# Kernel optimization log

Measured on AMD Instinct MI355X. Metric: run time of the kernel, lower is better.

The kernel has to match this reference:

```python
import jax, jax.numpy as jnp
import numpy as np

B, T, D, E, V, EXTRA = 32, 1024, 512, 256, 50257, 200


def setup_inputs() -> dict:
    key = jax.random.key(0)
    ks = jax.random.split(key, 20)
    s = 0.02
    rn = lambda k, shape: jax.random.normal(k, shape, dtype=jnp.float32) * s
    inp = {}
    inp["decoder_input"] = jax.random.randint(ks[0], (B,), 0, V)
    inp["h0"] = rn(ks[1], (B, D))
    inp["c0"] = rn(ks[2], (B, D))
    inp["encoder_outputs"] = rn(ks[3], (B, T, 2 * D))
    inp["encoder_pad_mask"] = jnp.ones((B, T), jnp.float32)
    inp["previous_context_vector"] = rn(ks[4], (B, 2 * D))
    inp["coverage"] = jax.random.uniform(ks[5], (B, T), jnp.float32) * 0.01
    inp["extra_zeros"] = jnp.zeros((B, EXTRA), jnp.float32)
    inp["encoder_input_extra_vocabs"] = jax.random.randint(ks[6], (B, T), 0, V + EXTRA)
    inp["step"] = 1
    inp["embedding"] = rn(ks[7], (V, E))
    inp["W_gx"] = rn(ks[8], (2 * D + E, E)); inp["b_gx"] = jnp.zeros((E,), jnp.float32)
    inp["W_ih"] = rn(ks[9], (E, 4 * D)); inp["W_hh"] = rn(ks[10], (D, 4 * D))
    inp["b_ih"] = jnp.zeros((4 * D,), jnp.float32); inp["b_hh"] = jnp.zeros((4 * D,), jnp.float32)
    inp["W_h"] = rn(ks[11], (2 * D, 2 * D))
    inp["W_c"] = rn(ks[12], (2 * D,))
    inp["W_s"] = rn(ks[13], (2 * D, 2 * D)); inp["b_s"] = jnp.zeros((2 * D,), jnp.float32)
    inp["v"] = rn(ks[14], (2 * D,))
    inp["W_pg"] = rn(ks[15], (4 * D + E,)); inp["b_pg"] = jnp.zeros((1,), jnp.float32)
    inp["W_v1"] = rn(ks[16], (3 * D, D)); inp["b_v1"] = jnp.zeros((D,), jnp.float32)
    inp["W_v2"] = rn(ks[17], (D, V)); inp["b_v2"] = jnp.zeros((V,), jnp.float32)
    return inp


def reference(decoder_input, h0, c0, encoder_outputs, encoder_pad_mask,
              previous_context_vector, coverage, extra_zeros,
              encoder_input_extra_vocabs, step,
              embedding, W_gx, b_gx, W_ih, W_hh, b_ih, b_hh,
              W_h, W_c, W_s, b_s, v, W_pg, b_pg, W_v1, b_v1, W_v2, b_v2):
    # Pointer-generator decoder single step (training path / step>0), coverage on.
    softmax_temperature = 1.0
    emb = embedding[decoder_input]                                  # [B,E]
    x = jnp.concatenate([previous_context_vector, emb], -1) @ W_gx + b_gx  # [B,E]
    # LSTM cell, torch gate order (i, f, g, o)
    gates = x @ W_ih + h0 @ W_hh + b_ih + b_hh                      # [B,4D]
    i, f, g, o = jnp.split(gates, 4, axis=-1)
    c1 = jax.nn.sigmoid(f) * c0 + jax.nn.sigmoid(i) * jnp.tanh(g)
    h1 = jax.nn.sigmoid(o) * jnp.tanh(c1)                           # [B,D]
    dec_hat = jnp.concatenate([h1, c1], -1)                         # [B,2D]
    # Bahdanau additive attention with coverage feature
    enc_feat = encoder_outputs @ W_h                                # [B,T,2D]
    dec_feat = dec_hat @ W_s + b_s                                  # [B,2D]
    cov_feat = coverage[..., None] * W_c                            # [B,T,2D]
    energy = jnp.tanh(enc_feat + dec_feat[:, None, :] + cov_feat)
    scores = energy @ v                                             # [B,T]
    att = jax.nn.softmax(scores / softmax_temperature, axis=-1) * encoder_pad_mask
    att = att / att.sum(-1, keepdims=True)                          # renormalized
    context = jnp.einsum('bt,btd->bd', att, encoder_outputs)        # [B,2D]
    coverage_next = coverage + att
    # pointer-generator gate
    pg_in = jnp.concatenate([context, dec_hat, x], -1)              # [B,4D+E]
    p_gen = jax.nn.sigmoid(pg_in @ W_pg + b_pg)[:, None]            # [B,1]
    out = jnp.concatenate([h1, context], -1)                        # [B,3D]
    logits = ((out @ W_v1 + b_v1) @ W_v2 + b_v2) / softmax_temperature
    vocab_dist = jax.nn.softmax(logits, axis=-1)                    # [B,V]
    vd_oov = jnp.concatenate([p_gen * vocab_dist, extra_zeros], 1)  # [B,V+EXTRA]
    att_oov = (1.0 - p_gen) * att                                   # [B,T]
    rows = jnp.arange(B)[:, None]
    vocab_dist_final = vd_oov.at[rows, encoder_input_extra_vocabs].add(att_oov)
    return (vocab_dist_final, (h1, c1), context, att, coverage_next)
```

## Files before the change

kernel.cpp:

```cpp
#include <hip/hip_runtime.h>
#include <hip/hip_bf16.h>

typedef __attribute__((ext_vector_type(4))) float f32x4;
typedef __attribute__((ext_vector_type(8))) short s16x8;
typedef __attribute__((ext_vector_type(4))) short s16x4;

#define DEVINL __device__ __forceinline__

static constexpr int BB = 32, TT = 1024, DD = 512, EE = 256, VV = 50257, EXTRA = 200;
static constexpr int D2 = 1024;
static constexpr int VE = VV + EXTRA;
static constexpr long MM = (long)BB * TT;
static constexpr int NBLK = 786;

DEVINL unsigned short f2bf(float x) {
    union { float f; unsigned int u; } c; c.f = x;
    unsigned int u = c.u;
    u += 0x7fffu + ((u >> 16) & 1u);
    return (unsigned short)(u >> 16);
}
DEVINL float bf2f(unsigned short h) {
    union { unsigned int u; float f; } c; c.u = ((unsigned int)h) << 16;
    return c.f;
}
DEVINL float sigmoidf_(float x) { return 1.0f / (1.0f + __expf(-x)); }
DEVINL float tanh_fast(float x) {
    x = fminf(15.f, fmaxf(-15.f, x));
    float e = __expf(2.f * x);
    return (e - 1.f) / (e + 1.f);
}
DEVINL void gl16(const void* g, void* l) {
    __builtin_amdgcn_global_load_lds((__attribute__((address_space(1))) void*)g,
                                     (__attribute__((address_space(3))) void*)l, 16, 0, 0);
}

__global__ __launch_bounds__(256) void k_prep(const float* __restrict__ Wh,
                                              const float* __restrict__ enc,
                                              unsigned short* __restrict__ WhT,
                                              unsigned short* __restrict__ encswz) {
    __shared__ float tile[32][33];
    const int bid = blockIdx.x, tid = threadIdx.x;
    if (bid < 1024) {
        int n0 = (bid & 31) * 32, k0 = (bid >> 5) * 32;
        int col = tid & 31, row = tid >> 5;
        #pragma unroll
        for (int i = 0; i < 4; i++)
            tile[row + i * 8][col] = Wh[(long)(k0 + row + i * 8) * D2 + n0 + col];
        __syncthreads();
        #pragma unroll
        for (int i = 0; i < 4; i++) {
            int n = n0 + row + i * 8;
            int kcol = (k0 + col) ^ ((n & 7) << 3);
            WhT[(long)n * D2 + kcol] = f2bf(tile[col][row + i * 8]);
        }
    } else {
        long idx = (long)(bid - 1024) * 256 + tid;
        int m  = (int)(idx >> 7);
        int k2 = (int)(idx & 127) * 8;
        int s  = (m & 7) << 3;
        const float* src = enc + (long)m * 1024 + (k2 ^ s);
        f32x4 a = *(const f32x4*)src;
        f32x4 b = *(const f32x4*)(src + 4);
        s16x8 h;
        h[0] = (short)f2bf(a[0]); h[1] = (short)f2bf(a[1]); h[2] = (short)f2bf(a[2]); h[3] = (short)f2bf(a[3]);
        h[4] = (short)f2bf(b[0]); h[5] = (short)f2bf(b[1]); h[6] = (short)f2bf(b[2]); h[7] = (short)f2bf(b[3]);
        *(s16x8*)(encswz + (long)m * 1024 + k2) = h;
    }
}

__global__ __launch_bounds__(512) void k_x(
    const int* __restrict__ dec_in, const float* __restrict__ pcv,
    const float* __restrict__ embt, const float* __restrict__ Wgx,
    const float* __restrict__ bgx, float* __restrict__ xbuf) {
    __shared__ float xs[1280];
    __shared__ float sred[8][64];
    int b = blockIdx.x, n0 = blockIdx.y * 64;
    int tid = threadIdx.x, nl = tid & 63, ks = tid >> 6;
    long er = (long)dec_in[b] * EE;
    for (int i = tid; i < 1280; i += 512)
        xs[i] = (i < 1024) ? pcv[b * 1024 + i] : embt[er + i - 1024];
    __syncthreads();
    float acc = 0.f;
    for (int k = ks * 160; k < ks * 160 + 160; ++k)
        acc += xs[k] * Wgx[(long)k * EE + n0 + nl];
    sred[ks][nl] = acc;
    __syncthreads();
    if (tid < 64) {
        int n = n0 + tid;
        float s = bgx[n];
        #pragma unroll
        for (int i = 0; i < 8; i++) s += sred[i][tid];
        xbuf[b * EE + n] = s;
    }
}

__global__ __launch_bounds__(512) void k_lstm(
    const float* __restrict__ xbuf, const float* __restrict__ h0,
    const float* __restrict__ c0, const float* __restrict__ Wih,
    const float* __restrict__ Whh, const float* __restrict__ bih,
    const float* __restrict__ bhh, float* __restrict__ h1o,
    float* __restrict__ c1o, float* __restrict__ dechat) {
    __shared__ float xs[768];
    __shared__ float sred[4][8][64];
    int b = blockIdx.x, d0 = blockIdx.y * 64;
    int tid = threadIdx.x, dl = tid & 63, ks = tid >> 6;
    for (int i = tid; i < 768; i += 512)
        xs[i] = (i < 256) ? xbuf[b * 256 + i] : h0[b * 512 + i - 256];
    __syncthreads();
    float a0 = 0, a1 = 0, a2 = 0, a3 = 0;
    for (int k = ks * 96; k < ks * 96 + 96; ++k) {
        float xv = xs[k];
        const float* wr = (k < 256) ? (Wih + (long)k * 2048) : (Whh + (long)(k - 256) * 2048);
        a0 += xv * wr[d0 + dl];        a1 += xv * wr[512 + d0 + dl];
        a2 += xv * wr[1024 + d0 + dl]; a3 += xv * wr[1536 + d0 + dl];
    }
    sred[0][ks][dl] = a0; sred[1][ks][dl] = a1; sred[2][ks][dl] = a2; sred[3][ks][dl] = a3;
    __syncthreads();
    if (tid < 64) {
        int d = d0 + tid;
        float gi = bih[d] + bhh[d];
        float gf = bih[512 + d] + bhh[512 + d];
        float gg = bih[1024 + d] + bhh[1024 + d];
        float go = bih[1536 + d] + bhh[1536 + d];
        #pragma unroll
        for (int s = 0; s < 8; s++) {
            gi += sred[0][s][tid]; gf += sred[1][s][tid];
            gg += sred[2][s][tid]; go += sred[3][s][tid];
        }
        float c1 = sigmoidf_(gf) * c0[b * 512 + d] + sigmoidf_(gi) * tanh_fast(gg);
        float h1 = sigmoidf_(go) * tanh_fast(c1);
        h1o[b * 512 + d] = h1; c1o[b * 512 + d] = c1;
        dechat[b * 1024 + d] = h1; dechat[b * 1024 + 512 + d] = c1;
    }
}

__global__ __launch_bounds__(512) void k_decfeat(
    const float* __restrict__ dechat, const float* __restrict__ Ws,
    const float* __restrict__ bs, float* __restrict__ decfeat) {
    __shared__ float xs[1024];
    __shared__ float sred[8][64];
    int b = blockIdx.x, n0 = blockIdx.y * 64;
    int tid = threadIdx.x, nl = tid & 63, ks = tid >> 6;
    for (int i = tid; i < 1024; i += 512) xs[i] = dechat[b * 1024 + i];
    __syncthreads();
    float acc = 0.f;
    for (int k = ks * 128; k < ks * 128 + 128; ++k)
        acc += xs[k] * Ws[(long)k * 1024 + n0 + nl];
    sred[ks][nl] = acc;
    __syncthreads();
    if (tid < 64) {
        int n = n0 + tid;
        float s = bs[n];
        #pragma unroll
        for (int i = 0; i < 8; i++) s += sred[i][tid];
        decfeat[b * 1024 + n] = s;
    }
}

__global__ __launch_bounds__(512) void k_scores(
    const unsigned short* __restrict__ encswz, const unsigned short* __restrict__ whtswz,
    const float* __restrict__ decfeat, const float* __restrict__ cov,
    const float* __restrict__ Wc, const float* __restrict__ vvec,
    float* __restrict__ scorep) {
    __shared__ __align__(16) unsigned short As[128 * 64];
    __shared__ __align__(16) unsigned short Bs[256 * 64];
    __shared__ float sred[4][128];
    const int tid = threadIdx.x;
    const int lane = tid & 63, wave = tid >> 6;
    const int wid = __builtin_amdgcn_readfirstlane(wave);
    const int g = lane >> 4, c = lane & 15;
    const int wm = wave >> 2, wn = wave & 3;

    const int bid = blockIdx.x;
    const int xcd = bid & 7, t = bid >> 3;
    const int mt = xcd * 32 + (t >> 2), nt = t & 3;
    const long m0 = (long)mt * 128;
    const int n0 = nt * 256;
    const int bblk = mt >> 3;

    const int arow = wid * 16 + (lane >> 3);
    const int axo  = (lane & 7) * 8;
    const int brow = wid * 32 + (lane >> 3);
    unsigned short* aBase = &As[wid * 1024];
    unsigned short* bBase = &Bs[wid * 2048];

    f32x4 acc[4][4];
    #pragma unroll
    for (int i = 0; i < 4; i++)
        #pragma unroll
        for (int j = 0; j < 4; j++) acc[i][j] = (f32x4){0.f, 0.f, 0.f, 0.f};

    const int sx = (c & 7) << 3;

    for (int kt = 0; kt < 16; ++kt) {
        const int k0 = kt * 64;
        __syncthreads();
        gl16(encswz + (m0 + arow) * 1024 + k0 + axo,       aBase);
        gl16(encswz + (m0 + arow + 8) * 1024 + k0 + axo,   aBase + 512);
        gl16(whtswz + (long)(n0 + brow) * 1024 + k0 + axo,        bBase);
        gl16(whtswz + (long)(n0 + brow + 8) * 1024 + k0 + axo,    bBase + 512);
        gl16(whtswz + (long)(n0 + brow + 16) * 1024 + k0 + axo,   bBase + 1024);
        gl16(whtswz + (long)(n0 + brow + 24) * 1024 + k0 + axo,   bBase + 1536);
        __syncthreads();
        #pragma unroll
        for (int kk = 0; kk < 2; ++kk) {
            const int kse = (kk * 32 + g * 8) ^ sx;
            s16x8 af[4], bfj[4];
            #pragma unroll
            for (int i = 0; i < 4; i++) af[i] = *(const s16x8*)&As[(wm * 64 + i * 16 + c) * 64 + kse];
            #pragma unroll
            for (int j = 0; j < 4; j++) bfj[j] = *(const s16x8*)&Bs[(wn * 64 + j * 16 + c) * 64 + kse];
            #pragma unroll
            for (int i = 0; i < 4; i++)
                #pragma unroll
                for (int j = 0; j < 4; j++)
                    acc[i][j] = __builtin_amdgcn_mfma_f32_16x16x32_bf16(af[i], bfj[j], acc[i][j], 0, 0, 0);
        }
    }
    float dfv[4], wcv[4], vvj[4];
    #pragma unroll
    for (int j = 0; j < 4; j++) {
        int col = n0 + wn * 64 + j * 16 + c;
        dfv[j] = decfeat[bblk * D2 + col];
        wcv[j] = Wc[col];
        vvj[j] = vvec[col];
    }
    float sAcc[4][4];
    #pragma unroll
    for (int i = 0; i < 4; i++) {
        #pragma unroll
        for (int r = 0; r < 4; r++) {
            const long m = m0 + wm * 64 + i * 16 + g * 4 + r;
            const float covm = cov[m];
            float su = 0.f;
            #pragma unroll
            for (int j = 0; j < 4; j++) {
                float e = acc[i][j][r] + dfv[j] + covm * wcv[j];
                su += tanh_fast(e) * vvj[j];
            }
            su += __shfl_xor(su, 1); su += __shfl_xor(su, 2);
            su += __shfl_xor(su, 4); su += __shfl_xor(su, 8);
            sAcc[i][r] = su;
        }
    }
    if (c == 0) {
        #pragma unroll
        for (int i = 0; i < 4; i++)
            #pragma unroll
            for (int r = 0; r < 4; r++)
                sred[wn][wm * 64 + i * 16 + g * 4 + r] = sAcc[i][r];
    }
    __syncthreads();
    if (tid < 128)
        scorep[(long)nt * MM + m0 + tid] = sred[0][tid] + sred[1][tid] + sred[2][tid] + sred[3][tid];
}

__global__ __launch_bounds__(256) void k_ctx(
    const float* __restrict__ scorep, const float* __restrict__ mask,
    const float* __restrict__ cov, const unsigned short* __restrict__ encswz,
    float* __restrict__ att, float* __restrict__ covn, float* __restrict__ part) {
    int b = blockIdx.x, tc = blockIdx.y;
    int tid = threadIdx.x;
    __shared__ float sm[8];
    __shared__ float attL[1024];
    float sv[4];
    float mx = -1e30f;
    #pragma unroll
    for (int i = 0; i < 4; i++) {
        long idx = (long)b * TT + tid + 256 * i;
        sv[i] = scorep[idx] + scorep[MM + idx] + scorep[2 * MM + idx] + scorep[3 * MM + idx];
        mx = fmaxf(mx, sv[i]);
    }
    for (int o = 32; o; o >>= 1) mx = fmaxf(mx, __shfl_xor(mx, o));
    if ((tid & 63) == 0) sm[tid >> 6] = mx;
    __syncthreads();
    mx = fmaxf(fmaxf(sm[0], sm[1]), fmaxf(sm[2], sm[3]));
    __syncthreads();
    float e[4]; float s = 0.f;
    #pragma unroll
    for (int i = 0; i < 4; i++) { e[i] = __expf(sv[i] - mx); s += e[i]; }
    for (int o = 32; o; o >>= 1) s += __shfl_xor(s, o);
    if ((tid & 63) == 0) sm[tid >> 6] = s;
    __syncthreads();
    s = sm[0] + sm[1] + sm[2] + sm[3];
    __syncthreads();
    float inv = 1.f / s;
    float am[4]; float s2 = 0.f;
    #pragma unroll
    for (int i = 0; i < 4; i++) { am[i] = e[i] * inv * mask[b * TT + tid + 256 * i]; s2 += am[i]; }
    for (int o = 32; o; o >>= 1) s2 += __shfl_xor(s2, o);
    if ((tid & 63) == 0) sm[tid >> 6] = s2;
    __syncthreads();
    s2 = sm[0] + sm[1] + sm[2] + sm[3];
    float inv2 = 1.f / s2;
    #pragma unroll
    for (int i = 0; i < 4; i++) {
        int t = tid + 256 * i;
        float a = am[i] * inv2;
        attL[t] = a;
        if (tc == 0) {
            att[b * TT + t] = a;
            covn[b * TT + t] = cov[b * TT + t] + a;
        }
    }
    __syncthreads();
    int d8 = (tid & 127) * 8;
    int tofs = tid >> 7;
    float a0 = 0, a1 = 0, a2 = 0, a3 = 0, a4 = 0, a5 = 0, a6 = 0, a7 = 0;
    for (int t = tc * 64 + tofs; t < tc * 64 + 64; t += 2) {
        float a = attL[t];
        int sx = (t & 7) << 3;
        const unsigned short* ep = encswz + ((long)b * TT + t) * D2 + (d8 ^ sx);
        s16x8 ev = *(const s16x8*)ep;
        a0 += a * bf2f((unsigned short)ev[0]); a1 += a * bf2f((unsigned short)ev[1]);
        a2 += a * bf2f((unsigned short)ev[2]); a3 += a * bf2f((unsigned short)ev[3]);
        a4 += a * bf2f((unsigned short)ev[4]); a5 += a * bf2f((unsigned short)ev[5]);
        a6 += a * bf2f((unsigned short)ev[6]); a7 += a * bf2f((unsigned short)ev[7]);
    }
    float* pp = part + (long)(tc * 2 + tofs) * BB * D2 + b * D2 + d8;
    pp[0] = a0; pp[1] = a1; pp[2] = a2; pp[3] = a3;
    pp[4] = a4; pp[5] = a5; pp[6] = a6; pp[7] = a7;
}

__global__ __launch_bounds__(512) void k_hidden2(
    const float* __restrict__ part, const float* __restrict__ h1,
    const float* __restrict__ dechat, const float* __restrict__ xbuf,
    const float* __restrict__ Wpg, const float* __restrict__ bpg,
    const float* __restrict__ Wv1, const float* __restrict__ bv1,
    float* __restrict__ ctx, float* __restrict__ pgen,
    unsigned short* __restrict__ hbf) {
    __shared__ float xs[1536];
    __shared__ float sred[8][64];
    int b = blockIdx.x, n0 = blockIdx.y * 64;
    int tid = threadIdx.x, nl = tid & 63, ks = tid >> 6;
    for (int i = tid; i < 512; i += 512) xs[i] = h1[b * 512 + i];
    #pragma unroll
    for (int d = tid; d < 1024; d += 512) {
        float s = 0.f;
        #pragma unroll
        for (int p = 0; p < 32; p++) s += part[(long)p * BB * D2 + b * D2 + d];
        xs[512 + d] = s;
        if (blockIdx.y == 0) ctx[b * D2 + d] = s;
    }
    __syncthreads();
    if (blockIdx.y == 0) {
        float pacc = xs[512 + tid] * Wpg[tid] + dechat[b * D2 + tid] * Wpg[D2 + tid]
                   + xs[1024 + tid] * Wpg[512 + tid] + dechat[b * D2 + 512 + tid] * Wpg[D2 + 512 + tid];
        if (tid < EE) pacc += xbuf[b * EE + tid] * Wpg[2 * D2 + tid];
        for (int o = 32; o; o >>= 1) pacc += __shfl_xor(pacc, o);
        if ((tid & 63) == 0) sred[7][(tid >> 6) + 8] = 0.f;
        __shared__ float psum[8];
        if ((tid & 63) == 0) psum[tid >> 6] = pacc;
        __syncthreads();
        if (tid == 0) {
            float t = 0.f;
            #pragma unroll
            for (int i = 0; i < 8; i++) t += psum[i];
            pgen[b] = sigmoidf_(t + bpg[0]);
        }
        __syncthreads();
    }
    float acc = 0.f;
    for (int k = ks * 192; k < ks * 192 + 192; ++k)
        acc += xs[k] * Wv1[(long)k * 512 + n0 + nl];
    sred[ks][nl] = acc;
    __syncthreads();
    if (tid < 64) {
        int n = n0 + tid;
        float s = bv1[n];
        #pragma unroll
        for (int i = 0; i < 8; i++) s += sred[i][tid];
        hbf[b * 512 + n] = f2bf(s);
    }
}

__global__ __launch_bounds__(256) void k_logits(const unsigned short* __restrict__ hbf,
                                                const float* __restrict__ Wv2,
                                                const float* __restrict__ bv2,
                                                float* __restrict__ logits,
                                                float* __restrict__ bsm,
                                                float* __restrict__ bss) {
    constexpr int PITCH = 136;
    __shared__ __align__(16) unsigned short Bs[64 * PITCH];
    __shared__ float sm_[4][16], ss_[4][16];
    const int tid = threadIdx.x;
    const int lane = tid & 63, wave = tid >> 6;
    const int g = lane >> 4, c = lane & 15;
    const int wm = wave >> 1, wn = wave & 1;
    const long v0 = (long)blockIdx.x * 64;
    const bool tail = (v0 + 64 > VV);

    const int vg = tid & 15, kr = tid >> 4;

    f32x4 acc[2];
    acc[0] = (f32x4){0.f, 0.f, 0.f, 0.f};
    acc[1] = (f32x4){0.f, 0.f, 0.f, 0.f};
    const int sxr = (c & 7) << 3;

    f32x4 wa[4], wb[4];
    #pragma unroll
    for (int pi = 0; pi < 4; ++pi) {
        const int ka = kr * 8 + pi * 2;
        if (!tail) {
            wa[pi] = *(const f32x4*)&Wv2[(long)ka * VV + v0 + vg * 4];
            wb[pi] = *(const f32x4*)&Wv2[(long)(ka + 1) * VV + v0 + vg * 4];
        } else {
            #pragma unroll
            for (int j = 0; j < 4; j++) {
                long v = v0 + vg * 4 + j;
                long vs = (v < VV) ? v : (VV - 1);
                wa[pi][j] = Wv2[(long)ka * VV + vs];
                wb[pi][j] = Wv2[(long)(ka + 1) * VV + vs];
            }
        }
    }
    #pragma unroll
    for (int kt = 0; kt < 4; ++kt) {
        const int k0 = kt * 128;
        __syncthreads();
        #pragma unroll
        for (int pi = 0; pi < 4; ++pi) {
            #pragma unroll
            for (int j = 0; j < 4; j++) {
                int vl = vg * 4 + j;
                int ks = (kr * 8 + pi * 2) ^ ((vl & 7) << 3);
                unsigned int pack = (unsigned int)f2bf(wa[pi][j]) | ((unsigned int)f2bf(wb[pi][j]) << 16);
                *(unsigned int*)&Bs[vl * PITCH + ks] = pack;
            }
        }
        if (kt < 3) {
            const int k1 = (kt + 1) * 128;
            #pragma unroll
            for (int pi = 0; pi < 4; ++pi) {
                const int ka = k1 + kr * 8 + pi * 2;
                if (!tail) {
                    wa[pi] = *(const f32x4*)&Wv2[(long)ka * VV + v0 + vg * 4];
                    wb[pi] = *(const f32x4*)&Wv2[(long)(ka + 1) * VV + v0 + vg * 4];
                } else {
                    #pragma unroll
                    for (int j = 0; j < 4; j++) {
                        long v = v0 + vg * 4 + j;
                        long vs = (v < VV) ? v : (VV - 1);
                        wa[pi][j] = Wv2[(long)ka * VV + vs];
                        wb[pi][j] = Wv2[(long)(ka + 1) * VV + vs];
                    }
                }
            }
        }
        __syncthreads();
        #pragma unroll
        for (int kk = 0; kk < 4; ++kk) {
            const int koff = kk * 32 + g * 8;
            const int kse = koff ^ sxr;
            s16x8 af = *(const s16x8*)&hbf[(wm * 16 + c) * 512 + k0 + koff];
            s16x8 bf0 = *(const s16x8*)&Bs[(wn * 32 + c) * PITCH + kse];
            s16x8 bf1 = *(const s16x8*)&Bs[(wn * 32 + 16 + c) * PITCH + kse];
            acc[0] = __builtin_amdgcn_mfma_f32_16x16x32_bf16(af, bf0, acc[0], 0, 0, 0);
            acc[1] = __builtin_amdgcn_mfma_f32_16x16x32_bf16(af, bf1, acc[1], 0, 0, 0);
        }
    }
    float lv[2][4];
    #pragma unroll
    for (int j = 0; j < 2; j++) {
        long v = v0 + wn * 32 + j * 16 + c;
        bool valid = (v < VV);
        float bvv = valid ? bv2[v] : 0.f;
        #pragma unroll
        for (int r = 0; r < 4; r++) {
            float val = acc[j][r] + bvv;
            if (valid) {
                int b = wm * 16 + g * 4 + r;
                logits[(long)b * VV + v] = val;
                lv[j][r] = val;
            } else {
                lv[j][r] = -1e30f;
            }
        }
    }
    float mrow[4], srow[4];
    #pragma unroll
    for (int r = 0; r < 4; r++) {
        float m = fmaxf(lv[0][r], lv[1][r]);
        m = fmaxf(m, __shfl_xor(m, 1)); m = fmaxf(m, __shfl_xor(m, 2));
        m = fmaxf(m, __shfl_xor(m, 4)); m = fmaxf(m, __shfl_xor(m, 8));
        float s = __expf(lv[0][r] - m) + __expf(lv[1][r] - m);
        s += __shfl_xor(s, 1); s += __shfl_xor(s, 2);
        s += __shfl_xor(s, 4); s += __shfl_xor(s, 8);
        mrow[r] = m; srow[r] = s;
    }
    if (c == 0) {
        #pragma unroll
        for (int r = 0; r < 4; r++) { sm_[wave][g * 4 + r] = mrow[r]; ss_[wave][g * 4 + r] = srow[r]; }
    }
    __syncthreads();
    if (tid < 32) {
        int b = tid;
        int w0 = (b >> 4) * 2, ridx = b & 15;
        float mA = sm_[w0][ridx], mB = sm_[w0 + 1][ridx];
        float sA = ss_[w0][ridx], sB = ss_[w0 + 1][ridx];
        float m = fmaxf(mA, mB);
        float s = sA * __expf(mA - m) + sB * __expf(mB - m);
        bsm[(long)b * NBLK + blockIdx.x] = m;
        bss[(long)b * NBLK + blockIdx.x] = s;
    }
}

__global__ __launch_bounds__(512) void k_vocab(
    const float* __restrict__ logits, const float* __restrict__ bsm,
    const float* __restrict__ bss, const float* __restrict__ pgen,
    const float* __restrict__ extraz, float* __restrict__ out0) {
    int b = blockIdx.x;
    int v0 = blockIdx.y * 2048;
    int tid = threadIdx.x;
    __shared__ float smm[8], sms[8], fin[2];
    float m = -1e30f, s = 0.f;
    #pragma unroll
    for (int it = 0; it < 2; ++it) {
        int i = tid + it * 512;
        if (i < NBLK) {
            float mi = bsm[(long)b * NBLK + i], si = bss[(long)b * NBLK + i];
            float nm = fmaxf(m, mi);
            s = s * __expf(m - nm) + si * __expf(mi - nm);
            m = nm;
        }
    }
    for (int o = 32; o; o >>= 1) {
        float m2 = __shfl_xor(m, o), s2 = __shfl_xor(s, o);
        float nm = fmaxf(m, m2);
        s = s * __expf(m - nm) + s2 * __expf(m2 - nm);
        m = nm;
    }
    if ((tid & 63) == 0) { smm[tid >> 6] = m; sms[tid >> 6] = s; }
    __syncthreads();
    if (tid == 0) {
        float fm = smm[0], fs = sms[0];
        #pragma unroll
        for (int i = 1; i < 8; i++) {
            float nm = fmaxf(fm, smm[i]);
            fs = fs * __expf(fm - nm) + sms[i] * __expf(smm[i] - nm);
            fm = nm;
        }
        fin[0] = fm; fin[1] = pgen[b] / fs;
    }
    __syncthreads();
    float mx = fin[0], inv = fin[1];
    const float* lr = logits + (long)b * VV;
    float* orow = out0 + (long)b * VE;
    #pragma unroll
    for (int i = 0; i < 4; i++) {
        int v = v0 + i * 512 + tid;
        if (v < VV)      orow[v] = __expf(lr[v] - mx) * inv;
        else if (v < VE) orow[v] = extraz[b * EXTRA + (v - VV)];
    }
}

__global__ __launch_bounds__(1024) void k_scatter(
    const int* __restrict__ eiv, const float* __restrict__ att,
    const float* __restrict__ pgen, float* __restrict__ out0) {
    int b = blockIdx.x, tid = threadIdx.x;
    float a = (1.f - pgen[b]) * att[b * TT + tid];
    atomicAdd(out0 + (long)b * VE + eiv[b * TT + tid], a);
}

extern "C" void kernel_launch(void* const* d_in, const int* in_sizes, int n_in,
                              void* d_out, int out_size, void* d_ws, size_t ws_size,
                              hipStream_t stream) {
    const int*   dec_in = (const int*)d_in[0];
    const float* h0     = (const float*)d_in[1];
    const float* c0     = (const float*)d_in[2];
    const float* enc    = (const float*)d_in[3];
    const float* mask   = (const float*)d_in[4];
    const float* pcv    = (const float*)d_in[5];
    const float* cov    = (const float*)d_in[6];
    const float* extraz = (const float*)d_in[7];
    const int*   eiv    = (const int*)d_in[8];
    const float* embt   = (const float*)d_in[10];
    const float* Wgx    = (const float*)d_in[11];
    const float* bgx    = (const float*)d_in[12];
    const float* Wih    = (const float*)d_in[13];
    const float* Whh    = (const float*)d_in[14];
    const float* bih    = (const float*)d_in[15];
    const float* bhh    = (const float*)d_in[16];
    const float* Wh     = (const float*)d_in[17];
    const float* Wc     = (const float*)d_in[18];
    const float* Ws     = (const float*)d_in[19];
    const float* bs     = (const float*)d_in[20];
    const float* vv     = (const float*)d_in[21];
    const float* Wpg    = (const float*)d_in[22];
    const float* bpg    = (const float*)d_in[23];
    const float* Wv1    = (const float*)d_in[24];
    const float* bv1    = (const float*)d_in[25];
    const float* Wv2    = (const float*)d_in[26];
    const float* bv2    = (const float*)d_in[27];

    float* out = (float*)d_out;
    float* out_vd  = out;
    float* out_h1  = out + (long)BB * VE;
    float* out_c1  = out_h1 + BB * DD;
    float* out_ctx = out_c1 + BB * DD;
    float* out_att = out_ctx + BB * D2;
    float* out_cov = out_att + BB * TT;

    char* p = (char*)d_ws;
    unsigned short* whtswz = (unsigned short*)p; p += (size_t)D2 * D2 * 2;
    float* xbuf    = (float*)p;  p += (size_t)BB * EE * 4;
    float* dechat  = (float*)p;  p += (size_t)BB * D2 * 4;
    float* decfeat = (float*)p;  p += (size_t)BB * D2 * 4;
    float* scorep  = (float*)p;  p += (size_t)4 * MM * 4;
    float* pgen    = (float*)p;  p += 256;
    unsigned short* hbf = (unsigned short*)p; p += (size_t)BB * DD * 2 + 256;
    float* bsm     = (float*)p;  p += (size_t)BB * NBLK * 4;
    float* bss     = (float*)p;  p += (size_t)BB * NBLK * 4;
    float* ctxpart = (float*)p;  p += (size_t)32 * BB * D2 * 4;
    float* logits  = (float*)p;  p += (size_t)BB * VV * 4;
    unsigned short* encswz = (unsigned short*)p; p += (size_t)MM * D2 * 2;

    k_prep<<<1024 + 16384, 256, 0, stream>>>(Wh, enc, whtswz, encswz);
    k_x<<<dim3(BB, 4), 512, 0, stream>>>(dec_in, pcv, embt, Wgx, bgx, xbuf);
    k_lstm<<<dim3(BB, 8), 512, 0, stream>>>(xbuf, h0, c0, Wih, Whh, bih, bhh, out_h1, out_c1, dechat);
    k_decfeat<<<dim3(BB, 16), 512, 0, stream>>>(dechat, Ws, bs, decfeat);
    k_scores<<<1024, 512, 0, stream>>>(encswz, whtswz, decfeat, cov, Wc, vv, scorep);
    k_ctx<<<dim3(BB, 16), 256, 0, stream>>>(scorep, mask, cov, encswz, out_att, out_cov, ctxpart);
    k_hidden2<<<dim3(BB, 8), 512, 0, stream>>>(ctxpart, out_h1, dechat, xbuf, Wpg, bpg,
                                               Wv1, bv1, out_ctx, pgen, hbf);
    k_logits<<<NBLK, 256, 0, stream>>>(hbf, Wv2, bv2, logits, bsm, bss);
    k_vocab<<<dim3(BB, 25), 512, 0, stream>>>(logits, bsm, bss, pgen, extraz, out_vd);
    k_scatter<<<BB, 1024, 0, stream>>>(eiv, out_att, pgen, out_vd);
}
```

Before: 234.0 us.

## Halve score GEMM N-tile and fold pointer scatter into vocab kernel

The attention score GEMM now uses 128x128 tiles instead of 128x256, which doubles the grid to 2048 blocks and the partial-score buffer to 8 slices. This cuts LDS and accumulator registers per block, aiming for better occupancy, at the cost of reloading the encoder tile twice as often. The separate scatter kernel is removed; each vocab block atomically adds the attention mass for target indices that fall in its own 2048-wide slice, which saves one launch but makes every block scan all 1024 indices. A stray shared-memory write in k_hidden2 is also dropped.

```diff
diff --git a/kernel.cpp b/kernel.cpp
--- a/kernel.cpp
+++ b/kernel.cpp
@@ -163,7 +163,7 @@
     const float* __restrict__ Wc, const float* __restrict__ vvec,
     float* __restrict__ scorep) {
     __shared__ __align__(16) unsigned short As[128 * 64];
-    __shared__ __align__(16) unsigned short Bs[256 * 64];
+    __shared__ __align__(16) unsigned short Bs[128 * 64];
     __shared__ float sred[4][128];
     const int tid = threadIdx.x;
     const int lane = tid & 63, wave = tid >> 6;
@@ -173,54 +173,51 @@
 
     const int bid = blockIdx.x;
     const int xcd = bid & 7, t = bid >> 3;
-    const int mt = xcd * 32 + (t >> 2), nt = t & 3;
+    const int mt = xcd * 32 + (t >> 3), nt = t & 7;
     const long m0 = (long)mt * 128;
-    const int n0 = nt * 256;
+    const int n0 = nt * 128;
     const int bblk = mt >> 3;
 
     const int arow = wid * 16 + (lane >> 3);
     const int axo  = (lane & 7) * 8;
-    const int brow = wid * 32 + (lane >> 3);
     unsigned short* aBase = &As[wid * 1024];
-    unsigned short* bBase = &Bs[wid * 2048];
-
-    f32x4 acc[4][4];
+    unsigned short* bBase = &Bs[wid * 1024];
+
+    f32x4 acc[4][2];
     #pragma unroll
     for (int i = 0; i < 4; i++)
         #pragma unroll
-        for (int j = 0; j < 4; j++) acc[i][j] = (f32x4){0.f, 0.f, 0.f, 0.f};
+        for (int j = 0; j < 2; j++) acc[i][j] = (f32x4){0.f, 0.f, 0.f, 0.f};
 
     const int sx = (c & 7) << 3;
 
     for (int kt = 0; kt < 16; ++kt) {
         const int k0 = kt * 64;
         __syncthreads();
-        gl16(encswz + (m0 + arow) * 1024 + k0 + axo,       aBase);
-        gl16(encswz + (m0 + arow + 8) * 1024 + k0 + axo,   aBase + 512);
-        gl16(whtswz + (long)(n0 + brow) * 1024 + k0 + axo,        bBase);
-        gl16(whtswz + (long)(n0 + brow + 8) * 1024 + k0 + axo,    bBase + 512);
-        gl16(whtswz + (long)(n0 + brow + 16) * 1024 + k0 + axo,   bBase + 1024);
-        gl16(whtswz + (long)(n0 + brow + 24) * 1024 + k0 + axo,   bBase + 1536);
+        gl16(encswz + (m0 + arow) * 1024 + k0 + axo,            aBase);
+        gl16(encswz + (m0 + arow + 8) * 1024 + k0 + axo,        aBase + 512);
+        gl16(whtswz + (long)(n0 + arow) * 1024 + k0 + axo,      bBase);
+        gl16(whtswz + (long)(n0 + arow + 8) * 1024 + k0 + axo,  bBase + 512);
         __syncthreads();
         #pragma unroll
         for (int kk = 0; kk < 2; ++kk) {
             const int kse = (kk * 32 + g * 8) ^ sx;
-            s16x8 af[4], bfj[4];
+            s16x8 af[4], bfj[2];
             #pragma unroll
             for (int i = 0; i < 4; i++) af[i] = *(const s16x8*)&As[(wm * 64 + i * 16 + c) * 64 + kse];
             #pragma unroll
-            for (int j = 0; j < 4; j++) bfj[j] = *(const s16x8*)&Bs[(wn * 64 + j * 16 + c) * 64 + kse];
+            for (int j = 0; j < 2; j++) bfj[j] = *(const s16x8*)&Bs[(wn * 32 + j * 16 + c) * 64 + kse];
             #pragma unroll
             for (int i = 0; i < 4; i++)
                 #pragma unroll
-                for (int j = 0; j < 4; j++)
+                for (int j = 0; j < 2; j++)
                     acc[i][j] = __builtin_amdgcn_mfma_f32_16x16x32_bf16(af[i], bfj[j], acc[i][j], 0, 0, 0);
         }
     }
-    float dfv[4], wcv[4], vvj[4];
-    #pragma unroll
-    for (int j = 0; j < 4; j++) {
-        int col = n0 + wn * 64 + j * 16 + c;
+    float dfv[2], wcv[2], vvj[2];
+    #pragma unroll
+    for (int j = 0; j < 2; j++) {
+        int col = n0 + wn * 32 + j * 16 + c;
         dfv[j] = decfeat[bblk * D2 + col];
         wcv[j] = Wc[col];
         vvj[j] = vvec[col];
@@ -234,7 +231,7 @@
             const float covm = cov[m];
             float su = 0.f;
             #pragma unroll
-            for (int j = 0; j < 4; j++) {
+            for (int j = 0; j < 2; j++) {
                 float e = acc[i][j][r] + dfv[j] + covm * wcv[j];
                 su += tanh_fast(e) * vvj[j];
             }
@@ -268,7 +265,10 @@
     #pragma unroll
     for (int i = 0; i < 4; i++) {
         long idx = (long)b * TT + tid + 256 * i;
-        sv[i] = scorep[idx] + scorep[MM + idx] + scorep[2 * MM + idx] + scorep[3 * MM + idx];
+        float s8 = 0.f;
+        #pragma unroll
+        for (int p = 0; p < 8; p++) s8 += scorep[(long)p * MM + idx];
+        sv[i] = s8;
         mx = fmaxf(mx, sv[i]);
     }
     for (int o = 32; o; o >>= 1) mx = fmaxf(mx, __shfl_xor(mx, o));
@@ -348,7 +348,6 @@
                    + xs[1024 + tid] * Wpg[512 + tid] + dechat[b * D2 + 512 + tid] * Wpg[D2 + 512 + tid];
         if (tid < EE) pacc += xbuf[b * EE + tid] * Wpg[2 * D2 + tid];
         for (int o = 32; o; o >>= 1) pacc += __shfl_xor(pacc, o);
-        if ((tid & 63) == 0) sred[7][(tid >> 6) + 8] = 0.f;
         __shared__ float psum[8];
         if ((tid & 63) == 0) psum[tid >> 6] = pacc;
         __syncthreads();
@@ -508,7 +507,8 @@
 __global__ __launch_bounds__(512) void k_vocab(
     const float* __restrict__ logits, const float* __restrict__ bsm,
     const float* __restrict__ bss, const float* __restrict__ pgen,
-    const float* __restrict__ extraz, float* __restrict__ out0) {
+    const float* __restrict__ extraz, const float* __restrict__ att,
+    const int* __restrict__ eiv, float* __restrict__ out0) {
     int b = blockIdx.x;
     int v0 = blockIdx.y * 2048;
     int tid = threadIdx.x;
@@ -544,6 +544,7 @@
     }
     __syncthreads();
     float mx = fin[0], inv = fin[1];
+    float pg = pgen[b];
     const float* lr = logits + (long)b * VV;
     float* orow = out0 + (long)b * VE;
     #pragma unroll
@@ -552,14 +553,17 @@
         if (v < VV)      orow[v] = __expf(lr[v] - mx) * inv;
         else if (v < VE) orow[v] = extraz[b * EXTRA + (v - VV)];
     }
-}
-
-__global__ __launch_bounds__(1024) void k_scatter(
-    const int* __restrict__ eiv, const float* __restrict__ att,
-    const float* __restrict__ pgen, float* __restrict__ out0) {
-    int b = blockIdx.x, tid = threadIdx.x;
-    float a = (1.f - pgen[b]) * att[b * TT + tid];
-    atomicAdd(out0 + (long)b * VE + eiv[b * TT + tid], a);
+    __syncthreads();
+    int vend = v0 + 2048;
+    #pragma unroll
+    for (int it = 0; it < 2; ++it) {
+        int t = tid + it * 512;
+        int tgt = eiv[b * TT + t];
+        if (tgt >= v0 && tgt < vend) {
+            float a = (1.f - pg) * att[b * TT + t];
+            atomicAdd(orow + tgt, a);
+        }
+    }
 }
 
 extern "C" void kernel_launch(void* const* d_in, const int* in_sizes, int n_in,
@@ -606,7 +610,7 @@
     float* xbuf    = (float*)p;  p += (size_t)BB * EE * 4;
     float* dechat  = (float*)p;  p += (size_t)BB * D2 * 4;
     float* decfeat = (float*)p;  p += (size_t)BB * D2 * 4;
-    float* scorep  = (float*)p;  p += (size_t)4 * MM * 4;
+    float* scorep  = (float*)p;  p += (size_t)8 * MM * 4;
     float* pgen    = (float*)p;  p += 256;
     unsigned short* hbf = (unsigned short*)p; p += (size_t)BB * DD * 2 + 256;
     float* bsm     = (float*)p;  p += (size_t)BB * NBLK * 4;
@@ -619,11 +623,10 @@
     k_x<<<dim3(BB, 4), 512, 0, stream>>>(dec_in, pcv, embt, Wgx, bgx, xbuf);
     k_lstm<<<dim3(BB, 8), 512, 0, stream>>>(xbuf, h0, c0, Wih, Whh, bih, bhh, out_h1, out_c1, dechat);
     k_decfeat<<<dim3(BB, 16), 512, 0, stream>>>(dechat, Ws, bs, decfeat);
-    k_scores<<<1024, 512, 0, stream>>>(encswz, whtswz, decfeat, cov, Wc, vv, scorep);
+    k_scores<<<2048, 512, 0, stream>>>(encswz, whtswz, decfeat, cov, Wc, vv, scorep);
     k_ctx<<<dim3(BB, 16), 256, 0, stream>>>(scorep, mask, cov, encswz, out_att, out_cov, ctxpart);
     k_hidden2<<<dim3(BB, 8), 512, 0, stream>>>(ctxpart, out_h1, dechat, xbuf, Wpg, bpg,
                                                Wv1, bv1, out_ctx, pgen, hbf);
     k_logits<<<NBLK, 256, 0, stream>>>(hbf, Wv2, bv2, logits, bsm, bss);
-    k_vocab<<<dim3(BB, 25), 512, 0, stream>>>(logits, bsm, bss, pgen, extraz, out_vd);
-    k_scatter<<<BB, 1024, 0, stream>>>(eiv, out_att, pgen, out_vd);
-}
+    k_vocab<<<dim3(BB, 25), 512, 0, stream>>>(logits, bsm, bss, pgen, extraz, out_att, eiv, out_vd);
+}
```

New measurement: 243.8 us. 1.04x slower.
